# Kernel tuning notes

Measured on AMD Instinct MI355X. Metric: run time of the kernel, lower is better.

Reference implementation:

```python
import jax, jax.numpy as jnp
import numpy as np

N, E, IN_DIM, EDGE_DIM, HID, OUT = 20000, 160000, 128, 32, 128, 64


def _p(key, shape):
    return jax.random.normal(key, shape, dtype=jnp.float32) * 0.05


def setup_inputs() -> dict:
    key = jax.random.key(0)
    ks = jax.random.split(key, 24)
    inp = {
        "x": jax.random.normal(ks[0], (N, IN_DIM), dtype=jnp.float32),
        "ei": jax.random.randint(ks[1], (2, E), 0, N, dtype=jnp.int64),
        "ea": jax.random.normal(ks[2], (E, EDGE_DIM), dtype=jnp.float32),
    }
    H1C1 = 4 * HID  # layer1: heads=4, out=HID, concat -> 512
    # layer 1 params (in=IN_DIM)
    inp["Wq1"] = _p(ks[3], (H1C1, IN_DIM)); inp["bq1"] = _p(ks[4], (H1C1,))
    inp["Wk1"] = _p(ks[5], (H1C1, IN_DIM)); inp["bk1"] = _p(ks[6], (H1C1,))
    inp["Wv1"] = _p(ks[7], (H1C1, IN_DIM)); inp["bv1"] = _p(ks[8], (H1C1,))
    inp["We1"] = _p(ks[9], (H1C1, EDGE_DIM))
    inp["Ws1"] = _p(ks[10], (H1C1, IN_DIM)); inp["bs1"] = _p(ks[11], (H1C1,))
    # layer 2 params (in=512, heads=1, out=OUT, concat=False)
    IN2 = H1C1
    inp["Wq2"] = _p(ks[12], (OUT, IN2)); inp["bq2"] = _p(ks[13], (OUT,))
    inp["Wk2"] = _p(ks[14], (OUT, IN2)); inp["bk2"] = _p(ks[15], (OUT,))
    inp["Wv2"] = _p(ks[16], (OUT, IN2)); inp["bv2"] = _p(ks[17], (OUT,))
    inp["We2"] = _p(ks[18], (OUT, EDGE_DIM))
    inp["Ws2"] = _p(ks[19], (OUT, IN2)); inp["bs2"] = _p(ks[20], (OUT,))
    return inp


def transformer_conv(x, ei, ea, Wq, bq, Wk, bk, Wv, bv, We, Ws, bs, heads, C, concat):
    """PyG TransformerConv: gather -> per-edge attention -> segment softmax -> scatter."""
    n = x.shape[0]
    src, dst = ei[0], ei[1]  # messages flow src -> dst
    q = (x @ Wq.T + bq).reshape(n, heads, C)
    k = (x @ Wk.T + bk).reshape(n, heads, C)
    v = (x @ Wv.T + bv).reshape(n, heads, C)
    e = (ea @ We.T).reshape(-1, heads, C)  # [E,H,C]
    kj = k[src] + e
    vj = v[src] + e
    alpha = jnp.einsum("ehc,ehc->eh", q[dst], kj) / jnp.sqrt(jnp.float32(C))
    # segment softmax over incoming edges of each dst node
    amax = jax.ops.segment_max(alpha, dst, num_segments=n)
    ex = jnp.exp(alpha - amax[dst])
    denom = jax.ops.segment_sum(ex, dst, num_segments=n)
    w = ex / denom[dst]  # [E,H]
    out = jax.ops.segment_sum(vj * w[:, :, None], dst, num_segments=n)  # [N,H,C]
    out = out.reshape(n, heads * C) if concat else out.mean(axis=1)
    return out + x @ Ws.T + bs  # root/skip connection


def reference(x, ei, ea,
              Wq1, bq1, Wk1, bk1, Wv1, bv1, We1, Ws1, bs1,
              Wq2, bq2, Wk2, bk2, Wv2, bv2, We2, Ws2, bs2):
    h = jax.nn.relu(transformer_conv(x, ei, ea, Wq1, bq1, Wk1, bk1, Wv1, bv1,
                                     We1, Ws1, bs1, heads=4, C=HID, concat=True))
    z = transformer_conv(h, ei, ea, Wq2, bq2, Wk2, bk2, Wv2, bv2,
                         We2, Ws2, bs2, heads=1, C=OUT, concat=False)
    return z
```

## Files before the change

kernel.cpp:

```cpp
#include <hip/hip_runtime.h>
#include <hip/hip_bf16.h>
#include <math.h>

#define N_NODES 20000
#define N_EDGES 160000
#define D1 512
#define D2 64
#define Y1W 2176
#define Y2W 288

typedef __attribute__((ext_vector_type(8))) short short8;
typedef __attribute__((ext_vector_type(4))) float floatx4;

__device__ __forceinline__ float bf2f(short u) {
    return __uint_as_float(((unsigned)(unsigned short)u) << 16);
}
__device__ __forceinline__ short f2bf(float f) {
    __hip_bfloat16 h = __float2bfloat16(f);
    return *(short*)&h;
}

__global__ void hist_kernel(const int* __restrict__ ei, int* __restrict__ deg) {
    int e = blockIdx.x * blockDim.x + threadIdx.x;
    if (e < N_EDGES) atomicAdd(&deg[ei[N_EDGES + e]], 1);
}

__global__ void scan_kernel(const int* __restrict__ deg, int* __restrict__ rowptr) {
    const int NT = 1024;
    const int CH = (N_NODES + NT - 1) / NT;
    __shared__ int sums[NT];
    int t = threadIdx.x;
    int base = t * CH;
    int s = 0;
    for (int i = 0; i < CH; ++i) {
        int idx = base + i;
        if (idx < N_NODES) s += deg[idx];
    }
    sums[t] = s;
    __syncthreads();
    for (int off = 1; off < NT; off <<= 1) {
        int v = (t >= off) ? sums[t - off] : 0;
        __syncthreads();
        sums[t] += v;
        __syncthreads();
    }
    int run = (t > 0) ? sums[t - 1] : 0;
    for (int i = 0; i < CH; ++i) {
        int idx = base + i;
        if (idx < N_NODES) {
            rowptr[idx] = run;
            run += deg[idx];
        }
    }
    if (t == NT - 1) rowptr[N_NODES] = sums[NT - 1];
}

__global__ void fill_kernel(const int* __restrict__ ei, const int* __restrict__ rowptr,
                            int* __restrict__ cursor, int2* __restrict__ e2) {
    int e = blockIdx.x * blockDim.x + threadIdx.x;
    if (e < N_EDGES) {
        int src = ei[e];
        int dst = ei[N_EDGES + e];
        int p = rowptr[dst] + atomicAdd(&cursor[dst], 1);
        e2[p] = make_int2(src, e);
    }
}

__global__ void prep1_kernel(const float* __restrict__ Wq1, const float* __restrict__ bq1,
                             const float* __restrict__ Wk1, const float* __restrict__ bk1,
                             const float* __restrict__ Wv1, const float* __restrict__ bv1,
                             const float* __restrict__ Ws1, const float* __restrict__ bs1,
                             const float* __restrict__ We1,
                             __hip_bfloat16* __restrict__ W1b, float* __restrict__ b1) {
    int j = blockIdx.x, t = threadIdx.x;
    if (j < 2048) {
        int sel = j >> 9, r = j & 511;
        const float* W = sel == 0 ? Wq1 : sel == 1 ? Wk1 : sel == 2 ? Wv1 : Ws1;
        const float* bs = sel == 0 ? bq1 : sel == 1 ? bk1 : sel == 2 ? bv1 : bs1;
        W1b[(size_t)j * 128 + t] = __float2bfloat16(W[(size_t)r * 128 + t]);
        if (t == 0) b1[j] = bs[r];
    } else {
        int hd = j - 2048, h = hd >> 5, d = hd & 31;
        float acc = 0.f;
        for (int c = 0; c < 128; ++c)
            acc += Wq1[(size_t)(h * 128 + c) * 128 + t] * We1[(size_t)(h * 128 + c) * 32 + d];
        W1b[(size_t)j * 128 + t] = __float2bfloat16(acc);
        if (t == 0) {
            float b = 0.f;
            for (int c = 0; c < 128; ++c) b += bq1[h * 128 + c] * We1[(size_t)(h * 128 + c) * 32 + d];
            b1[j] = b;
        }
    }
}

__global__ void prep2_kernel(const float* __restrict__ Wq2, const float* __restrict__ bq2,
                             const float* __restrict__ Wk2, const float* __restrict__ bk2,
                             const float* __restrict__ Wv2, const float* __restrict__ bv2,
                             const float* __restrict__ Ws2, const float* __restrict__ bs2,
                             const float* __restrict__ We2,
                             __hip_bfloat16* __restrict__ W2b, float* __restrict__ b2) {
    int j = blockIdx.x, t = threadIdx.x;
    for (int kk = t; kk < 512; kk += 256) {
        float val;
        if (j < 256) {
            int sel = j >> 6, r = j & 63;
            const float* W = sel == 0 ? Wq2 : sel == 1 ? Wk2 : sel == 2 ? Wv2 : Ws2;
            val = W[(size_t)r * 512 + kk];
        } else {
            int d = j - 256;
            float acc = 0.f;
            for (int c = 0; c < 64; ++c) acc += Wq2[(size_t)c * 512 + kk] * We2[c * 32 + d];
            val = acc;
        }
        W2b[(size_t)j * 512 + kk] = __float2bfloat16(val);
    }
    if (t == 0) {
        if (j < 256) {
            int sel = j >> 6, r = j & 63;
            const float* bs = sel == 0 ? bq2 : sel == 1 ? bk2 : sel == 2 ? bv2 : bs2;
            b2[j] = bs[r];
        } else {
            int d = j - 256;
            float b = 0.f;
            for (int c = 0; c < 64; ++c) b += bq2[c] * We2[c * 32 + d];
            b2[j] = b;
        }
    }
}

template <int K, bool A_F32, bool OUT_BF16>
__global__ __launch_bounds__(256) void gemm_bt(const void* __restrict__ Ap,
                                               const __hip_bfloat16* __restrict__ B,
                                               const float* __restrict__ bias,
                                               void* __restrict__ Cout,
                                               int M, int N, int tiles_n) {
    __shared__ char lds[65536];
    char* ldsA = lds;
    char* ldsB = lds + 32768;
    int tid = threadIdx.x;
    int bm = blockIdx.x / tiles_n, bn = blockIdx.x % tiles_n;
    int w = tid >> 6, lane = tid & 63;
    int wr = (w >> 1) * 64, wc = (w & 1) * 64;
    int lrow = lane & 15, lk = lane >> 4;
    floatx4 acc[4][4] = {};

    for (int kt = 0; kt < K / 128; ++kt) {
        if (kt) __syncthreads();
        #pragma unroll
        for (int it = 0; it < 8; ++it) {
            int s = it * 256 + tid;
            int row = s >> 4, kslot = s & 15;
            int phys = ((kslot ^ (row & 15)) << 4);
            int gr = bm * 128 + row;
            if (gr > M - 1) gr = M - 1;
            short8 va;
            if (A_F32) {
                const float* Af = (const float*)Ap;
                float4 x0 = *(const float4*)(Af + (size_t)gr * K + kt * 128 + kslot * 8);
                float4 x1 = *(const float4*)(Af + (size_t)gr * K + kt * 128 + kslot * 8 + 4);
                va[0] = f2bf(x0.x); va[1] = f2bf(x0.y); va[2] = f2bf(x0.z); va[3] = f2bf(x0.w);
                va[4] = f2bf(x1.x); va[5] = f2bf(x1.y); va[6] = f2bf(x1.z); va[7] = f2bf(x1.w);
            } else {
                const __hip_bfloat16* Ab = (const __hip_bfloat16*)Ap;
                va = *(const short8*)(Ab + (size_t)gr * K + kt * 128 + kslot * 8);
            }
            *(short8*)(ldsA + row * 256 + phys) = va;
            int gc = bn * 128 + row;
            if (gc > N - 1) gc = N - 1;
            short8 vb = *(const short8*)(B + (size_t)gc * K + kt * 128 + kslot * 8);
            *(short8*)(ldsB + row * 256 + phys) = vb;
        }
        __syncthreads();
        #pragma unroll
        for (int ks = 0; ks < 4; ++ks) {
            short8 af[4], bfr[4];
            #pragma unroll
            for (int m = 0; m < 4; ++m) {
                int r = wr + m * 16 + lrow;
                int kslot = ks * 4 + lk;
                af[m] = *(const short8*)(ldsA + r * 256 + ((kslot ^ (r & 15)) << 4));
            }
            #pragma unroll
            for (int n = 0; n < 4; ++n) {
                int c = wc + n * 16 + lrow;
                int kslot = ks * 4 + lk;
                bfr[n] = *(const short8*)(ldsB + c * 256 + ((kslot ^ (c & 15)) << 4));
            }
            #pragma unroll
            for (int m = 0; m < 4; ++m)
                #pragma unroll
                for (int n = 0; n < 4; ++n)
                    acc[m][n] = __builtin_amdgcn_mfma_f32_16x16x32_bf16(af[m], bfr[n], acc[m][n], 0, 0, 0);
        }
    }

    #pragma unroll
    for (int m = 0; m < 4; ++m) {
        #pragma unroll
        for (int j = 0; j < 4; ++j) {
            int r = bm * 128 + wr + m * 16 + lk * 4 + j;
            if (r >= M) continue;
            #pragma unroll
            for (int n = 0; n < 4; ++n) {
                int gc = bn * 128 + wc + n * 16 + lrow;
                if (gc >= N) continue;
                float v = acc[m][n][j] + bias[gc];
                if (OUT_BF16)
                    ((__hip_bfloat16*)Cout)[(size_t)r * N + gc] = __float2bfloat16(v);
                else
                    ((float*)Cout)[(size_t)r * N + gc] = v;
            }
        }
    }
}

__global__ __launch_bounds__(256) void attn1_kernel(
    const __hip_bfloat16* __restrict__ Y1, const float* __restrict__ ea,
    const int2* __restrict__ e2, const int* __restrict__ rowptr,
    const float* __restrict__ We1, __hip_bfloat16* __restrict__ hb) {
    int wid = threadIdx.x >> 6, lane = threadIdx.x & 63;
    int dst = blockIdx.x * 4 + wid;
    if (dst >= N_NODES) return;
    int c0 = lane * 8;
    int hh = lane >> 4;
    int d0 = (lane & 15) * 2;
    const size_t rowb = (size_t)dst * Y1W;
    short8 qv = *(const short8*)(Y1 + rowb + c0);
    float q[8];
    #pragma unroll
    for (int j = 0; j < 8; ++j) q[j] = bf2f(qv[j]);
    const __hip_bfloat16* pp = Y1 + rowb + 2048 + hh * 32 + d0;
    float pA = __bfloat162float(pp[0]);
    float pB = __bfloat162float(pp[1]);

    float acc[8] = {0.f, 0.f, 0.f, 0.f, 0.f, 0.f, 0.f, 0.f};
    float t0 = 0.f, t1 = 0.f, denom = 0.f;
    int beg = rowptr[dst], end = rowptr[dst + 1];

    auto proc = [&](short8 kv, short8 vv, float ea0, float ea1) {
        float s = pA * ea0 + pB * ea1;
        #pragma unroll
        for (int j = 0; j < 8; ++j) s += q[j] * bf2f(kv[j]);
        s += __shfl_xor(s, 1);
        s += __shfl_xor(s, 2);
        s += __shfl_xor(s, 4);
        s += __shfl_xor(s, 8);
        float wgt = __expf(s * 0.08838834764831845f);
        denom += wgt;
        #pragma unroll
        for (int j = 0; j < 8; ++j) acc[j] += wgt * bf2f(vv[j]);
        t0 += wgt * ea0;
        t1 += wgt * ea1;
    };

    int i = beg;
    for (; i + 2 <= end; i += 2) {
        int2 eA = e2[i], eB = e2[i + 1];
        const size_t ra = (size_t)eA.x * Y1W, rb = (size_t)eB.x * Y1W;
        short8 kA = *(const short8*)(Y1 + ra + 512 + c0);
        short8 kB = *(const short8*)(Y1 + rb + 512 + c0);
        short8 vA = *(const short8*)(Y1 + ra + 1024 + c0);
        short8 vB = *(const short8*)(Y1 + rb + 1024 + c0);
        float2 fA = *(const float2*)(ea + (size_t)eA.y * 32 + d0);
        float2 fB = *(const float2*)(ea + (size_t)eB.y * 32 + d0);
        proc(kA, vA, fA.x, fA.y);
        proc(kB, vB, fB.x, fB.y);
    }
    if (i < end) {
        int2 eA = e2[i];
        const size_t ra = (size_t)eA.x * Y1W;
        short8 kA = *(const short8*)(Y1 + ra + 512 + c0);
        short8 vA = *(const short8*)(Y1 + ra + 1024 + c0);
        float2 fA = *(const float2*)(ea + (size_t)eA.y * 32 + d0);
        proc(kA, vA, fA.x, fA.y);
    }

    float tt[32];
    int gbase = lane & 48;
    #pragma unroll
    for (int d = 0; d < 32; ++d)
        tt[d] = __shfl((d & 1) ? t1 : t0, gbase + (d >> 1));
    float inv = (end > beg) ? 1.f / denom : 0.f;
    short8 sv = *(const short8*)(Y1 + rowb + 1536 + c0);
    short8 hv;
    #pragma unroll
    for (int j = 0; j < 8; ++j) {
        const float4* wr = (const float4*)(We1 + (size_t)(c0 + j) * 32);
        float sum = 0.f;
        #pragma unroll
        for (int d4 = 0; d4 < 8; ++d4) {
            float4 w4 = wr[d4];
            sum += w4.x * tt[d4 * 4] + w4.y * tt[d4 * 4 + 1]
                 + w4.z * tt[d4 * 4 + 2] + w4.w * tt[d4 * 4 + 3];
        }
        float v = (acc[j] + sum) * inv + bf2f(sv[j]);
        hv[j] = f2bf(v > 0.f ? v : 0.f);
    }
    *(short8*)(hb + (size_t)dst * D1 + c0) = hv;
}

__global__ __launch_bounds__(256) void attn2_kernel(
    const float* __restrict__ Y2, const float* __restrict__ ea,
    const int2* __restrict__ e2, const int* __restrict__ rowptr,
    const float* __restrict__ We2, float* __restrict__ zout) {
    int wid = threadIdx.x >> 6, lane = threadIdx.x & 63;
    int dst = blockIdx.x * 4 + wid;
    if (dst >= N_NODES) return;
    const size_t rowb = (size_t)dst * Y2W;
    float qv = Y2[rowb + lane];
    float pv = (lane < 32) ? Y2[rowb + 256 + lane] : 0.f;
    float acc = 0.f, t = 0.f, denom = 0.f;
    int beg = rowptr[dst], end = rowptr[dst + 1];

    auto proc = [&](float kv, float vv, float eav) {
        float s = qv * kv + pv * eav;
        s += __shfl_xor(s, 1);
        s += __shfl_xor(s, 2);
        s += __shfl_xor(s, 4);
        s += __shfl_xor(s, 8);
        s += __shfl_xor(s, 16);
        s += __shfl_xor(s, 32);
        float wgt = __expf(s * 0.125f);
        denom += wgt;
        acc += wgt * vv;
        t += wgt * eav;
    };

    int i = beg;
    for (; i + 2 <= end; i += 2) {
        int2 eA = e2[i], eB = e2[i + 1];
        const size_t ra = (size_t)eA.x * Y2W, rb = (size_t)eB.x * Y2W;
        float kA = Y2[ra + 64 + lane], kB = Y2[rb + 64 + lane];
        float vA = Y2[ra + 128 + lane], vB = Y2[rb + 128 + lane];
        float eaA = (lane < 32) ? ea[(size_t)eA.y * 32 + lane] : 0.f;
        float eaB = (lane < 32) ? ea[(size_t)eB.y * 32 + lane] : 0.f;
        proc(kA, vA, eaA);
        proc(kB, vB, eaB);
    }
    if (i < end) {
        int2 eA = e2[i];
        const size_t ra = (size_t)eA.x * Y2W;
        proc(Y2[ra + 64 + lane], Y2[ra + 128 + lane],
             (lane < 32) ? ea[(size_t)eA.y * 32 + lane] : 0.f);
    }

    float tt[32];
    #pragma unroll
    for (int d = 0; d < 32; ++d) tt[d] = __shfl(t, d);
    float inv = (end > beg) ? 1.f / denom : 0.f;
    const float4* wr = (const float4*)(We2 + (size_t)lane * 32);
    float sum = 0.f;
    #pragma unroll
    for (int d4 = 0; d4 < 8; ++d4) {
        float4 w4 = wr[d4];
        sum += w4.x * tt[d4 * 4] + w4.y * tt[d4 * 4 + 1]
             + w4.z * tt[d4 * 4 + 2] + w4.w * tt[d4 * 4 + 3];
    }
    zout[(size_t)dst * D2 + lane] = (acc + sum) * inv + Y2[rowb + 192 + lane];
}

extern "C" void kernel_launch(void* const* d_in, const int* in_sizes, int n_in,
                              void* d_out, int out_size, void* d_ws, size_t ws_size,
                              hipStream_t stream) {
    const float* x   = (const float*)d_in[0];
    const int*   ei  = (const int*)d_in[1];
    const float* ea  = (const float*)d_in[2];
    const float* Wq1 = (const float*)d_in[3];  const float* bq1 = (const float*)d_in[4];
    const float* Wk1 = (const float*)d_in[5];  const float* bk1 = (const float*)d_in[6];
    const float* Wv1 = (const float*)d_in[7];  const float* bv1 = (const float*)d_in[8];
    const float* We1 = (const float*)d_in[9];
    const float* Ws1 = (const float*)d_in[10]; const float* bs1 = (const float*)d_in[11];
    const float* Wq2 = (const float*)d_in[12]; const float* bq2 = (const float*)d_in[13];
    const float* Wk2 = (const float*)d_in[14]; const float* bk2 = (const float*)d_in[15];
    const float* Wv2 = (const float*)d_in[16]; const float* bv2 = (const float*)d_in[17];
    const float* We2 = (const float*)d_in[18];
    const float* Ws2 = (const float*)d_in[19]; const float* bs2 = (const float*)d_in[20];
    float* zout = (float*)d_out;

    char* wsb = (char*)d_ws;
    size_t off = 0;
    auto alloc = [&](size_t bytes) -> void* {
        void* p = wsb + off;
        off += (bytes + 255) & ~(size_t)255;
        return p;
    };
    __hip_bfloat16* Y1  = (__hip_bfloat16*)alloc((size_t)N_NODES * Y1W * 2);
    __hip_bfloat16* hbb = (__hip_bfloat16*)alloc((size_t)N_NODES * D1 * 2);
    float*          Y2  = (float*)alloc((size_t)N_NODES * Y2W * 4);
    __hip_bfloat16* W1b = (__hip_bfloat16*)alloc((size_t)2176 * 128 * 2);
    float*          b1  = (float*)alloc(2176 * 4);
    __hip_bfloat16* W2b = (__hip_bfloat16*)alloc((size_t)288 * 512 * 2);
    float*          b2  = (float*)alloc(288 * 4);
    int* deg    = (int*)alloc((size_t)N_NODES * 4);
    int* cursor = (int*)alloc((size_t)N_NODES * 4);
    int* rowptr = (int*)alloc((size_t)(N_NODES + 1) * 4);
    int2* e2    = (int2*)alloc((size_t)N_EDGES * 8);

    hipMemsetAsync(deg, 0, (size_t)N_NODES * 4, stream);
    hipMemsetAsync(cursor, 0, (size_t)N_NODES * 4, stream);

    hist_kernel<<<(N_EDGES + 255) / 256, 256, 0, stream>>>(ei, deg);
    scan_kernel<<<1, 1024, 0, stream>>>(deg, rowptr);
    fill_kernel<<<(N_EDGES + 255) / 256, 256, 0, stream>>>(ei, rowptr, cursor, e2);

    prep1_kernel<<<2176, 128, 0, stream>>>(Wq1, bq1, Wk1, bk1, Wv1, bv1, Ws1, bs1,
                                           We1, W1b, b1);
    prep2_kernel<<<288, 256, 0, stream>>>(Wq2, bq2, Wk2, bk2, Wv2, bv2, Ws2, bs2,
                                          We2, W2b, b2);

    int tiles_m = (N_NODES + 127) / 128;
    gemm_bt<128, true, true><<<tiles_m * 17, 256, 0, stream>>>(
        (const void*)x, W1b, b1, (void*)Y1, N_NODES, Y1W, 17);
    attn1_kernel<<<(N_NODES + 3) / 4, 256, 0, stream>>>(Y1, ea, e2, rowptr, We1, hbb);

    gemm_bt<512, false, false><<<tiles_m * 3, 256, 0, stream>>>(
        (const void*)hbb, W2b, b2, (void*)Y2, N_NODES, Y2W, 3);
    attn2_kernel<<<(N_NODES + 3) / 4, 256, 0, stream>>>(Y2, ea, e2, rowptr, We2, zout);
}
```

Before: 549.7 us.

## Permute edge attrs into CSR order, batch 8 edge gathers, store Y2 in bf16

Adds a kernel that permutes edge attributes into destination-sorted CSR order, so the attention kernels read them contiguously instead of through an edge-id indirection. Both attention kernels now issue loads for up to 8 edges before computing, which raises memory-level parallelism on the gathered K/V rows. The layer-2 GEMM output is stored as bf16, halving gather traffic in attn2. The cost is an extra permutation pass writing about 20 MB, plus some precision loss in layer-2 projections.

```diff
diff --git a/kernel.cpp b/kernel.cpp
--- a/kernel.cpp
+++ b/kernel.cpp
@@ -56,14 +56,24 @@
 }
 
 __global__ void fill_kernel(const int* __restrict__ ei, const int* __restrict__ rowptr,
-                            int* __restrict__ cursor, int2* __restrict__ e2) {
+                            int* __restrict__ cursor, int* __restrict__ srcs,
+                            int* __restrict__ eid) {
     int e = blockIdx.x * blockDim.x + threadIdx.x;
     if (e < N_EDGES) {
         int src = ei[e];
         int dst = ei[N_EDGES + e];
         int p = rowptr[dst] + atomicAdd(&cursor[dst], 1);
-        e2[p] = make_int2(src, e);
-    }
+        srcs[p] = src;
+        eid[p] = e;
+    }
+}
+
+__global__ void eaperm_kernel(const float* __restrict__ ea, const int* __restrict__ eid,
+                              float* __restrict__ eap) {
+    int idx = blockIdx.x * 256 + threadIdx.x;
+    if (idx >= N_EDGES * 32) return;
+    int p = idx >> 5, d = idx & 31;
+    eap[idx] = ea[(size_t)eid[p] * 32 + d];
 }
 
 __global__ void prep1_kernel(const float* __restrict__ Wq1, const float* __restrict__ bq1,
@@ -215,8 +225,8 @@
 }
 
 __global__ __launch_bounds__(256) void attn1_kernel(
-    const __hip_bfloat16* __restrict__ Y1, const float* __restrict__ ea,
-    const int2* __restrict__ e2, const int* __restrict__ rowptr,
+    const __hip_bfloat16* __restrict__ Y1, const float* __restrict__ eap,
+    const int* __restrict__ srcs, const int* __restrict__ rowptr,
     const float* __restrict__ We1, __hip_bfloat16* __restrict__ hb) {
     int wid = threadIdx.x >> 6, lane = threadIdx.x & 63;
     int dst = blockIdx.x * 4 + wid;
@@ -237,42 +247,42 @@
     float t0 = 0.f, t1 = 0.f, denom = 0.f;
     int beg = rowptr[dst], end = rowptr[dst + 1];
 
-    auto proc = [&](short8 kv, short8 vv, float ea0, float ea1) {
-        float s = pA * ea0 + pB * ea1;
-        #pragma unroll
-        for (int j = 0; j < 8; ++j) s += q[j] * bf2f(kv[j]);
-        s += __shfl_xor(s, 1);
-        s += __shfl_xor(s, 2);
-        s += __shfl_xor(s, 4);
-        s += __shfl_xor(s, 8);
-        float wgt = __expf(s * 0.08838834764831845f);
-        denom += wgt;
-        #pragma unroll
-        for (int j = 0; j < 8; ++j) acc[j] += wgt * bf2f(vv[j]);
-        t0 += wgt * ea0;
-        t1 += wgt * ea1;
-    };
-
-    int i = beg;
-    for (; i + 2 <= end; i += 2) {
-        int2 eA = e2[i], eB = e2[i + 1];
-        const size_t ra = (size_t)eA.x * Y1W, rb = (size_t)eB.x * Y1W;
-        short8 kA = *(const short8*)(Y1 + ra + 512 + c0);
-        short8 kB = *(const short8*)(Y1 + rb + 512 + c0);
-        short8 vA = *(const short8*)(Y1 + ra + 1024 + c0);
-        short8 vB = *(const short8*)(Y1 + rb + 1024 + c0);
-        float2 fA = *(const float2*)(ea + (size_t)eA.y * 32 + d0);
-        float2 fB = *(const float2*)(ea + (size_t)eB.y * 32 + d0);
-        proc(kA, vA, fA.x, fA.y);
-        proc(kB, vB, fB.x, fB.y);
-    }
-    if (i < end) {
-        int2 eA = e2[i];
-        const size_t ra = (size_t)eA.x * Y1W;
-        short8 kA = *(const short8*)(Y1 + ra + 512 + c0);
-        short8 vA = *(const short8*)(Y1 + ra + 1024 + c0);
-        float2 fA = *(const float2*)(ea + (size_t)eA.y * 32 + d0);
-        proc(kA, vA, fA.x, fA.y);
+    for (int i = beg; i < end; i += 8) {
+        int n = end - i;
+        if (n > 8) n = 8;
+        int sr[8];
+        float2 ff[8];
+        short8 kk[8], vv[8];
+        #pragma unroll
+        for (int j = 0; j < 8; ++j)
+            if (j < n) {
+                sr[j] = srcs[i + j];
+                ff[j] = *(const float2*)(eap + (size_t)(i + j) * 32 + d0);
+            }
+        #pragma unroll
+        for (int j = 0; j < 8; ++j)
+            if (j < n) {
+                const __hip_bfloat16* rp = Y1 + (size_t)sr[j] * Y1W;
+                kk[j] = *(const short8*)(rp + 512 + c0);
+                vv[j] = *(const short8*)(rp + 1024 + c0);
+            }
+        #pragma unroll
+        for (int j = 0; j < 8; ++j)
+            if (j < n) {
+                float s = pA * ff[j].x + pB * ff[j].y;
+                #pragma unroll
+                for (int c = 0; c < 8; ++c) s += q[c] * bf2f(kk[j][c]);
+                s += __shfl_xor(s, 1);
+                s += __shfl_xor(s, 2);
+                s += __shfl_xor(s, 4);
+                s += __shfl_xor(s, 8);
+                float wgt = __expf(s * 0.08838834764831845f);
+                denom += wgt;
+                #pragma unroll
+                for (int c = 0; c < 8; ++c) acc[c] += wgt * bf2f(vv[j][c]);
+                t0 += wgt * ff[j].x;
+                t1 += wgt * ff[j].y;
+            }
     }
 
     float tt[32];
@@ -300,48 +310,52 @@
 }
 
 __global__ __launch_bounds__(256) void attn2_kernel(
-    const float* __restrict__ Y2, const float* __restrict__ ea,
-    const int2* __restrict__ e2, const int* __restrict__ rowptr,
+    const __hip_bfloat16* __restrict__ Y2, const float* __restrict__ eap,
+    const int* __restrict__ srcs, const int* __restrict__ rowptr,
     const float* __restrict__ We2, float* __restrict__ zout) {
     int wid = threadIdx.x >> 6, lane = threadIdx.x & 63;
     int dst = blockIdx.x * 4 + wid;
     if (dst >= N_NODES) return;
     const size_t rowb = (size_t)dst * Y2W;
-    float qv = Y2[rowb + lane];
-    float pv = (lane < 32) ? Y2[rowb + 256 + lane] : 0.f;
+    float qv = __bfloat162float(Y2[rowb + lane]);
+    float pv = (lane < 32) ? __bfloat162float(Y2[rowb + 256 + lane]) : 0.f;
     float acc = 0.f, t = 0.f, denom = 0.f;
     int beg = rowptr[dst], end = rowptr[dst + 1];
 
-    auto proc = [&](float kv, float vv, float eav) {
-        float s = qv * kv + pv * eav;
-        s += __shfl_xor(s, 1);
-        s += __shfl_xor(s, 2);
-        s += __shfl_xor(s, 4);
-        s += __shfl_xor(s, 8);
-        s += __shfl_xor(s, 16);
-        s += __shfl_xor(s, 32);
-        float wgt = __expf(s * 0.125f);
-        denom += wgt;
-        acc += wgt * vv;
-        t += wgt * eav;
-    };
-
-    int i = beg;
-    for (; i + 2 <= end; i += 2) {
-        int2 eA = e2[i], eB = e2[i + 1];
-        const size_t ra = (size_t)eA.x * Y2W, rb = (size_t)eB.x * Y2W;
-        float kA = Y2[ra + 64 + lane], kB = Y2[rb + 64 + lane];
-        float vA = Y2[ra + 128 + lane], vB = Y2[rb + 128 + lane];
-        float eaA = (lane < 32) ? ea[(size_t)eA.y * 32 + lane] : 0.f;
-        float eaB = (lane < 32) ? ea[(size_t)eB.y * 32 + lane] : 0.f;
-        proc(kA, vA, eaA);
-        proc(kB, vB, eaB);
-    }
-    if (i < end) {
-        int2 eA = e2[i];
-        const size_t ra = (size_t)eA.x * Y2W;
-        proc(Y2[ra + 64 + lane], Y2[ra + 128 + lane],
-             (lane < 32) ? ea[(size_t)eA.y * 32 + lane] : 0.f);
+    for (int i = beg; i < end; i += 8) {
+        int n = end - i;
+        if (n > 8) n = 8;
+        int sr[8];
+        float ff[8];
+        short kb[8], vb[8];
+        #pragma unroll
+        for (int j = 0; j < 8; ++j)
+            if (j < n) {
+                sr[j] = srcs[i + j];
+                ff[j] = (lane < 32) ? eap[(size_t)(i + j) * 32 + lane] : 0.f;
+            }
+        #pragma unroll
+        for (int j = 0; j < 8; ++j)
+            if (j < n) {
+                const __hip_bfloat16* rp = Y2 + (size_t)sr[j] * Y2W;
+                kb[j] = *(const short*)(rp + 64 + lane);
+                vb[j] = *(const short*)(rp + 128 + lane);
+            }
+        #pragma unroll
+        for (int j = 0; j < 8; ++j)
+            if (j < n) {
+                float s = qv * bf2f(kb[j]) + pv * ff[j];
+                s += __shfl_xor(s, 1);
+                s += __shfl_xor(s, 2);
+                s += __shfl_xor(s, 4);
+                s += __shfl_xor(s, 8);
+                s += __shfl_xor(s, 16);
+                s += __shfl_xor(s, 32);
+                float wgt = __expf(s * 0.125f);
+                denom += wgt;
+                acc += wgt * bf2f(vb[j]);
+                t += wgt * ff[j];
+            }
     }
 
     float tt[32];
@@ -356,7 +370,8 @@
         sum += w4.x * tt[d4 * 4] + w4.y * tt[d4 * 4 + 1]
              + w4.z * tt[d4 * 4 + 2] + w4.w * tt[d4 * 4 + 3];
     }
-    zout[(size_t)dst * D2 + lane] = (acc + sum) * inv + Y2[rowb + 192 + lane];
+    zout[(size_t)dst * D2 + lane] =
+        (acc + sum) * inv + __bfloat162float(Y2[rowb + 192 + lane]);
 }
 
 extern "C" void kernel_launch(void* const* d_in, const int* in_sizes, int n_in,
@@ -386,7 +401,7 @@
     };
     __hip_bfloat16* Y1  = (__hip_bfloat16*)alloc((size_t)N_NODES * Y1W * 2);
     __hip_bfloat16* hbb = (__hip_bfloat16*)alloc((size_t)N_NODES * D1 * 2);
-    float*          Y2  = (float*)alloc((size_t)N_NODES * Y2W * 4);
+    __hip_bfloat16* Y2  = (__hip_bfloat16*)alloc((size_t)N_NODES * Y2W * 2);
     __hip_bfloat16* W1b = (__hip_bfloat16*)alloc((size_t)2176 * 128 * 2);
     float*          b1  = (float*)alloc(2176 * 4);
     __hip_bfloat16* W2b = (__hip_bfloat16*)alloc((size_t)288 * 512 * 2);
@@ -394,14 +409,17 @@
     int* deg    = (int*)alloc((size_t)N_NODES * 4);
     int* cursor = (int*)alloc((size_t)N_NODES * 4);
     int* rowptr = (int*)alloc((size_t)(N_NODES + 1) * 4);
-    int2* e2    = (int2*)alloc((size_t)N_EDGES * 8);
+    int* srcs   = (int*)alloc((size_t)N_EDGES * 4);
+    int* eid    = (int*)alloc((size_t)N_EDGES * 4);
+    float* eap  = (float*)alloc((size_t)N_EDGES * 32 * 4);
 
     hipMemsetAsync(deg, 0, (size_t)N_NODES * 4, stream);
     hipMemsetAsync(cursor, 0, (size_t)N_NODES * 4, stream);
 
     hist_kernel<<<(N_EDGES + 255) / 256, 256, 0, stream>>>(ei, deg);
     scan_kernel<<<1, 1024, 0, stream>>>(deg, rowptr);
-    fill_kernel<<<(N_EDGES + 255) / 256, 256, 0, stream>>>(ei, rowptr, cursor, e2);
+    fill_kernel<<<(N_EDGES + 255) / 256, 256, 0, stream>>>(ei, rowptr, cursor, srcs, eid);
+    eaperm_kernel<<<(N_EDGES * 32 + 255) / 256, 256, 0, stream>>>(ea, eid, eap);
 
     prep1_kernel<<<2176, 128, 0, stream>>>(Wq1, bq1, Wk1, bk1, Wv1, bv1, Ws1, bs1,
                                            We1, W1b, b1);
@@ -411,9 +429,9 @@
     int tiles_m = (N_NODES + 127) / 128;
     gemm_bt<128, true, true><<<tiles_m * 17, 256, 0, stream>>>(
         (const void*)x, W1b, b1, (void*)Y1, N_NODES, Y1W, 17);
-    attn1_kernel<<<(N_NODES + 3) / 4, 256, 0, stream>>>(Y1, ea, e2, rowptr, We1, hbb);
-
-    gemm_bt<512, false, false><<<tiles_m * 3, 256, 0, stream>>>(
+    attn1_kernel<<<(N_NODES + 3) / 4, 256, 0, stream>>>(Y1, eap, srcs, rowptr, We1, hbb);
+
+    gemm_bt<512, false, true><<<tiles_m * 3, 256, 0, stream>>>(
         (const void*)hbb, W2b, b2, (void*)Y2, N_NODES, Y2W, 3);
-    attn2_kernel<<<(N_NODES + 3) / 4, 256, 0, stream>>>(Y2, ea, e2, rowptr, We2, zout);
-}
+    attn2_kernel<<<(N_NODES + 3) / 4, 256, 0, stream>>>(Y2, eap, srcs, rowptr, We2, zout);
+}
```

Result: slower. 629.2 us (+14.5%).
